# Performance work log

Measured on AMD Instinct MI355X. Metric: run time of the kernel, lower is better.

Reference implementation:

```python
import math
import jax, jax.numpy as jnp
import numpy as np

B, S, HID, NH = 2, 2048, 2048, 16
HD = HID // NH          # 128
QKD = HD // 2           # 64
BASE = 10000.0
LAYER_ID = 1
LAMBDA_INIT = 0.8 - 0.6 * math.exp(-0.3 * LAYER_ID)
EPS = 1e-6


def _rope_tables():
    i = np.arange(0, HD, 2, dtype=np.float32)
    theta = BASE ** (-i / HD)                      # [HD/2]
    pos = np.arange(S, dtype=np.float32)
    m_theta = np.outer(pos, theta)                 # [S, HD/2]
    cos = np.repeat(np.cos(m_theta), 2, axis=1)    # [S, HD]
    sin = np.repeat(np.sin(m_theta), 2, axis=1)
    return jnp.asarray(cos), jnp.asarray(sin)


def setup_inputs() -> dict:
    key = jax.random.key(0)
    ks = jax.random.split(key, 12)
    wstd = 0.02
    cos_emb, sin_emb = _rope_tables()
    return {
        "q": jax.random.normal(ks[0], (B, S, HID), jnp.float32),
        "k": jax.random.normal(ks[1], (B, S, HID), jnp.float32),
        "v": jax.random.normal(ks[2], (B, S, HID), jnp.float32),
        "Wq": jax.random.normal(ks[3], (HID, HID), jnp.float32) * wstd,
        "Wk": jax.random.normal(ks[4], (HID, HID), jnp.float32) * wstd,
        "Wv": jax.random.normal(ks[5], (HID, HID), jnp.float32) * wstd,
        "Wo": jax.random.normal(ks[6], (HID, HID), jnp.float32) * wstd,
        "lambda_q1": jax.random.normal(ks[7], (HD,), jnp.float32) * 0.1,
        "lambda_k1": jax.random.normal(ks[8], (HD,), jnp.float32) * 0.1,
        "lambda_q2": jax.random.normal(ks[9], (HD,), jnp.float32) * 0.1,
        "lambda_k2": jax.random.normal(ks[10], (HD,), jnp.float32) * 0.1,
        "gnorm_w": jnp.ones((HD,), jnp.float32),
        "cos_emb": cos_emb,
        "sin_emb": sin_emb,
        "mask": jnp.triu(jnp.ones((S, S), bool), 1),  # causal: True = masked
    }


def _apply_rope(x, cos_emb, sin_emb):
    # x: [B, 2, H, S, QKD]; tables sliced to [:S, :QKD] as in the torch code
    cos = cos_emb[:S, :QKD][None, None, None]
    sin = sin_emb[:S, :QKD][None, None, None]
    inv = jnp.stack((-x[..., 1::2], x[..., 0::2]), axis=-1).reshape(x.shape)
    return x * cos + inv * sin


def reference(q, k, v, Wq, Wk, Wv, Wo, lambda_q1, lambda_k1, lambda_q2,
              lambda_k2, gnorm_w, cos_emb, sin_emb, mask):
    lin = lambda x, W: jnp.einsum('bsi,oi->bso', x, W)  # torch Linear: x @ W.T
    qh = lin(q, Wq).reshape(B, S, NH, 2, QKD).transpose(0, 3, 2, 1, 4)  # [B,2,H,S,QKD]
    kh = lin(k, Wk).reshape(B, S, NH, 2, QKD).transpose(0, 3, 2, 1, 4)
    vh = lin(v, Wv).reshape(B, S, NH, HD).transpose(0, 2, 1, 3)          # [B,H,S,HD]
    qh = _apply_rope(qh, cos_emb, sin_emb)
    kh = _apply_rope(kh, cos_emb, sin_emb)

    scores = jnp.einsum('bghsd,bghtd->bghst', qh, kh) / math.sqrt(QKD)   # [B,2,H,S,S]
    scores = jnp.where(mask, jnp.finfo(jnp.float32).min, scores)

    lam1 = jnp.exp(jnp.sum(lambda_q1 * lambda_k1))
    lam2 = jnp.exp(jnp.sum(lambda_q2 * lambda_k2))
    lam = lam1 - lam2 + LAMBDA_INIT

    attn = jax.nn.softmax(scores[:, 0], axis=-1) - lam * jax.nn.softmax(scores[:, 1], axis=-1)
    out = jnp.einsum('bhst,bhtd->bhsd', attn, vh)                        # [B,H,S,HD]

    rms = out * jax.lax.rsqrt(jnp.mean(out * out, axis=-1, keepdims=True) + EPS) * gnorm_w
    out = (1.0 - LAMBDA_INIT) * rms
    out = out.transpose(0, 2, 1, 3).reshape(B, S, HID)
    return lin(out, Wo)
```

## Files before the change

kernel.cpp:

```cpp
#include <hip/hip_runtime.h>
#include <math.h>

#define BDIM 2
#define SDIM 2048
#define HIDD 2048
#define NHH 16
#define HDD 128
#define QKDD 64
#define MTOT (BDIM*SDIM)

constexpr float LAMBDA_INIT_F = 0.3555090675909693f;
constexpr float EPS_F = 1e-6f;
constexpr float SCALE_F = 0.125f;

typedef float f32x4 __attribute__((ext_vector_type(4)));
typedef short bf16x8 __attribute__((ext_vector_type(8)));
typedef short bf16x4 __attribute__((ext_vector_type(4)));

#define MFMA16(a, b, c) __builtin_amdgcn_mfma_f32_16x16x32_bf16((a), (b), (c), 0, 0, 0)

__device__ __forceinline__ short f2bf(float f) {
    unsigned u = __float_as_uint(f);
    u += 0x7FFFu + ((u >> 16) & 1u);
    return (short)(u >> 16);
}
__device__ __forceinline__ unsigned pk2(float a, float b) {
    return (unsigned)(unsigned short)f2bf(a) | ((unsigned)(unsigned short)f2bf(b) << 16);
}

__device__ __forceinline__ void gload_lds16(const void* g, void* l) {
    __builtin_amdgcn_global_load_lds(
        (const __attribute__((address_space(1))) void*)g,
        (__attribute__((address_space(3))) void*)l, 16, 0, 0);
}

__global__ void lambda_kernel(const float* __restrict__ lq1, const float* __restrict__ lk1,
                              const float* __restrict__ lq2, const float* __restrict__ lk2,
                              float* __restrict__ lam_out) {
    int l = threadIdx.x;
    float d1 = lq1[l] * lk1[l] + lq1[l + 64] * lk1[l + 64];
    float d2 = lq2[l] * lk2[l] + lq2[l + 64] * lk2[l + 64];
#pragma unroll
    for (int o = 32; o > 0; o >>= 1) {
        d1 += __shfl_down(d1, o);
        d2 += __shfl_down(d2, o);
    }
    if (l == 0) lam_out[0] = expf(d1) - expf(d2) + LAMBDA_INIT_F;
}

__global__ __launch_bounds__(256) void conv_x(const float* __restrict__ s0,
                                              const float* __restrict__ s1,
                                              const float* __restrict__ s2,
                                              short* __restrict__ dst, int n) {
    const float* src = (blockIdx.y == 0) ? s0 : (blockIdx.y == 1) ? s1 : s2;
    short* out = dst + (size_t)blockIdx.y * n;
    int i = (blockIdx.x * 256 + threadIdx.x) * 8;
    if (i >= n) return;
    float4 a = *(const float4*)&src[i];
    float4 b = *(const float4*)&src[i + 4];
    uint4 o;
    o.x = pk2(a.x, a.y); o.y = pk2(a.z, a.w);
    o.z = pk2(b.x, b.y); o.w = pk2(b.z, b.w);
    *(uint4*)&out[i] = o;
}
__global__ __launch_bounds__(256) void conv_w(const float* __restrict__ s0,
                                              const float* __restrict__ s1,
                                              const float* __restrict__ s2,
                                              const float* __restrict__ s3,
                                              short* __restrict__ dst, int n) {
    const float* src = (blockIdx.y == 0) ? s0 : (blockIdx.y == 1) ? s1
                     : (blockIdx.y == 2) ? s2 : s3;
    short* out = dst + (size_t)blockIdx.y * n;
    int i = (blockIdx.x * 256 + threadIdx.x) * 8;
    if (i >= n) return;
    float4 a = *(const float4*)&src[i];
    float4 b = *(const float4*)&src[i + 4];
    uint4 o;
    o.x = pk2(a.x, a.y); o.y = pk2(a.z, a.w);
    o.z = pk2(b.x, b.y); o.w = pk2(b.z, b.w);
    *(uint4*)&out[i] = o;
}

#define GK 2048

__device__ __forceinline__ void gemm_mainloop(
        const short* __restrict__ X, const short* __restrict__ W,
        short* As, short* Bs, f32x4 acc[4][4],
        int bm, int bn, int w, int l, int lq, int lg, int wr, int wc) {
    const int scol = (((l & 7) ^ (l >> 3)) << 3);
    const int rsw  = (lq & 7) << 3;
    const short* aS[4]; const short* bS[4];
    short* aD[4]; short* bD[4];
#pragma unroll
    for (int i = 0; i < 4; ++i) {
        const int c = w * 4 + i;
        aS[i] = X + (size_t)(bm + c * 8 + (l >> 3)) * GK + scol;
        bS[i] = W + (size_t)(bn + c * 8 + (l >> 3)) * GK + scol;
        aD[i] = As + c * 512;
        bD[i] = Bs + c * 512;
    }
    for (int k0 = 0; k0 < GK; k0 += 64) {
        __syncthreads();
#pragma unroll
        for (int i = 0; i < 4; ++i) {
            gload_lds16(aS[i] + k0, aD[i]);
            gload_lds16(bS[i] + k0, bD[i]);
        }
        __syncthreads();
#pragma unroll
        for (int kk = 0; kk < 2; ++kk) {
            bf16x8 a[4], b[4];
#pragma unroll
            for (int m = 0; m < 4; ++m)
                a[m] = *(const bf16x8*)&As[(wr * 64 + m * 16 + lq) * 64 + ((kk * 32 + lg * 8) ^ rsw)];
#pragma unroll
            for (int n = 0; n < 4; ++n)
                b[n] = *(const bf16x8*)&Bs[(wc * 64 + n * 16 + lq) * 64 + ((kk * 32 + lg * 8) ^ rsw)];
#pragma unroll
            for (int m = 0; m < 4; ++m)
#pragma unroll
                for (int n = 0; n < 4; ++n)
                    acc[m][n] = MFMA16(a[m], b[n], acc[m][n]);
        }
    }
}

__global__ __launch_bounds__(256) void qkv_gemm(
        const short* __restrict__ Xq, const short* __restrict__ Xk, const short* __restrict__ Xv,
        const short* __restrict__ Wb, short* __restrict__ Qb, short* __restrict__ Kb,
        short* __restrict__ Vb, const float* __restrict__ cosE, const float* __restrict__ sinE) {
    __shared__ short As[128 * 64];
    __shared__ short Bs[128 * 64];
    const int tid = threadIdx.x;
    const int w = tid >> 6, l = tid & 63;
    const int lq = l & 15, lg = l >> 4;
    const int wr = w >> 1, wc = w & 1;
    const int bm = blockIdx.y * 128;
    const int bn = blockIdx.x * 128;
    const int z  = blockIdx.z;

    const short* X = (z == 0) ? Xq : (z == 1) ? Xk : Xv;
    const short* W = Wb + (size_t)z * HIDD * HIDD;
    short* Cb      = (z == 0) ? Qb : (z == 1) ? Kb : Vb;

    f32x4 acc[4][4] = {};
    gemm_mainloop(X, W, As, Bs, acc, bm, bn, w, l, lq, lg, wr, wc);

    const bool dorope = (z < 2);
#pragma unroll
    for (int m = 0; m < 4; ++m)
#pragma unroll
        for (int n = 0; n < 4; ++n) {
            const int row0 = bm + wr * 64 + m * 16 + lg * 4;
            const int col  = bn + wc * 64 + n * 16 + lq;
#pragma unroll
            for (int r = 0; r < 4; ++r) {
                float vv = acc[m][n][r];
                if (dorope) {
                    const int s  = (row0 + r) & (SDIM - 1);
                    const int c6 = col & 63;
                    const float cv = cosE[s * HDD + c6];
                    const float sv = sinE[s * HDD + c6];
                    const float p = __shfl_xor(vv, 1);
                    vv = (col & 1) ? vv * cv + p * sv : vv * cv - p * sv;
                }
                Cb[(size_t)(row0 + r) * HIDD + col] = f2bf(vv);
            }
        }
}

__global__ __launch_bounds__(256) void o_gemm(const short* __restrict__ Ab,
                                              const short* __restrict__ Bb,
                                              float* __restrict__ C) {
    __shared__ short As[128 * 64];
    __shared__ short Bs[128 * 64];
    const int tid = threadIdx.x;
    const int w = tid >> 6, l = tid & 63;
    const int lq = l & 15, lg = l >> 4;
    const int wr = w >> 1, wc = w & 1;
    const int bm = blockIdx.y * 128;
    const int bn = blockIdx.x * 128;

    f32x4 acc[4][4] = {};
    gemm_mainloop(Ab, Bb, As, Bs, acc, bm, bn, w, l, lq, lg, wr, wc);

#pragma unroll
    for (int m = 0; m < 4; ++m)
#pragma unroll
        for (int n = 0; n < 4; ++n) {
            const int row0 = bm + wr * 64 + m * 16 + lg * 4;
            const int col  = bn + wc * 64 + n * 16 + lq;
#pragma unroll
            for (int r = 0; r < 4; ++r)
                C[(size_t)(row0 + r) * HIDD + col] = acc[m][n][r];
        }
}

#define KVB 64

__device__ __forceinline__ bf16x8 pack_pa(const float p0[4], const float p1[4]) {
    union { unsigned u[4]; bf16x8 v; } r;
    r.u[0] = pk2(p0[0], p0[1]);
    r.u[1] = pk2(p0[2], p0[3]);
    r.u[2] = pk2(p1[0], p1[1]);
    r.u[3] = pk2(p1[2], p1[3]);
    return r.v;
}

__device__ __forceinline__ void softmax_step(
        f32x4 sc[4], float& M, float& L, f32x4 O[8], bf16x8 pa[2],
        int t0, int qg, int lg, bool domask) {
#pragma unroll
    for (int sub = 0; sub < 4; ++sub)
#pragma unroll
        for (int r = 0; r < 4; ++r) {
            float s = sc[sub][r] * SCALE_F;
            if (domask) {
                int key = t0 + sub * 16 + lg * 4 + r;
                s = (key <= qg) ? s : -1e30f;
            }
            sc[sub][r] = s;
        }
    float mx = -1e30f;
#pragma unroll
    for (int sub = 0; sub < 4; ++sub) {
        float a01 = fmaxf(sc[sub][0], sc[sub][1]);
        float a23 = fmaxf(sc[sub][2], sc[sub][3]);
        mx = fmaxf(mx, fmaxf(a01, a23));
    }
    mx = fmaxf(mx, __shfl_xor(mx, 16));
    mx = fmaxf(mx, __shfl_xor(mx, 32));
    if (__ballot(mx > M + 8.f)) {
        const float Mn = fmaxf(M, mx);
        const float a = __expf(M - Mn);
        M = Mn;
        L *= a;
        float ar[4];
#pragma unroll
        for (int r = 0; r < 4; ++r) ar[r] = __shfl(a, lg * 4 + r);
#pragma unroll
        for (int d = 0; d < 8; ++d) {
            O[d][0] *= ar[0]; O[d][1] *= ar[1]; O[d][2] *= ar[2]; O[d][3] *= ar[3];
        }
    }
    float p[4][4];
    float ps = 0.f;
#pragma unroll
    for (int sub = 0; sub < 4; ++sub) {
#pragma unroll
        for (int r = 0; r < 4; ++r) p[sub][r] = __expf(sc[sub][r] - M);
        ps += (p[sub][0] + p[sub][1]) + (p[sub][2] + p[sub][3]);
    }
    ps += __shfl_xor(ps, 16);
    ps += __shfl_xor(ps, 32);
    L += ps;
    pa[0] = pack_pa(p[0], p[1]);
    pa[1] = pack_pa(p[2], p[3]);
}

__global__ __launch_bounds__(256, 2) void flash_mfma(
        const short* __restrict__ Qb, const short* __restrict__ Kb,
        const short* __restrict__ Vb, const float* __restrict__ gnw,
        const float* __restrict__ lam_p, short* __restrict__ Hob) {
    __shared__ short Ksh[KVB * 128];
    __shared__ short VT[HDD * 72];

    const int tid = threadIdx.x;
    const int w  = tid >> 6;
    const int l  = tid & 63;
    const int lq = l & 15;
    const int lg = l >> 4;

    const int blk = blockIdx.x;
    const int bh  = blk & 31;
    const int bx  = 31 - (blk >> 5);
    const int b = bh >> 4, h = bh & 15;
    const int s0 = bx * 64;
    const float lam = lam_p[0];

    const int qg = s0 + w * 16 + lq;
    const short* qrow = Qb + ((size_t)(b * SDIM + qg)) * HIDD + h * HDD;
    bf16x8 qf[2][2];
#pragma unroll
    for (int br = 0; br < 2; ++br)
#pragma unroll
        for (int ks = 0; ks < 2; ++ks)
            qf[br][ks] = *(const bf16x8*)(qrow + br * 64 + ks * 32 + lg * 8);

    int kkey[4], kcol[4];
#pragma unroll
    for (int i = 0; i < 4; ++i) {
        kkey[i] = w * 16 + i * 4 + lg;
        kcol[i] = (lq * 8) ^ ((kkey[i] & 7) << 3);
    }
    const int kp = tid & 31, dq = tid >> 5;

    const short* Kbase = Kb + ((size_t)(b * SDIM)) * HIDD + h * HDD;
    const short* Vbase = Vb + ((size_t)(b * SDIM)) * HIDD + h * HDD;

    float M1 = -1e30f, M2 = -1e30f, L1 = 0.f, L2 = 0.f;
    f32x4 O1[8] = {}; f32x4 O2[8] = {};

    const int ntmax = bx + 1;
    const int qmin = s0 + w * 16;
    const int ntw = (qmin >> 6) + 1;

    for (int t = 0; t < ntmax; ++t) {
        const size_t trow = (size_t)t * KVB * HIDD;
        __syncthreads();
#pragma unroll
        for (int i = 0; i < 4; ++i)
            gload_lds16(Kbase + trow + (size_t)kkey[i] * HIDD + kcol[i],
                        &Ksh[w * 2048 + i * 512]);
        {
            const short* v0 = Vbase + trow + (size_t)(2 * kp) * HIDD + dq * 16;
            const short* v1 = v0 + HIDD;
            bf16x8 v00 = *(const bf16x8*)v0;
            bf16x8 v01 = *(const bf16x8*)(v0 + 8);
            bf16x8 v10 = *(const bf16x8*)v1;
            bf16x8 v11 = *(const bf16x8*)(v1 + 8);
#pragma unroll
            for (int j = 0; j < 8; ++j) {
                unsigned ua = (unsigned)(unsigned short)v00[j] |
                              ((unsigned)(unsigned short)v10[j] << 16);
                *(unsigned*)&VT[(dq * 16 + j) * 72 + 2 * kp] = ua;
                unsigned ub = (unsigned)(unsigned short)v01[j] |
                              ((unsigned)(unsigned short)v11[j] << 16);
                *(unsigned*)&VT[(dq * 16 + 8 + j) * 72 + 2 * kp] = ub;
            }
        }
        __syncthreads();
        if (t >= ntw) continue;

        f32x4 sc1[4] = {}; f32x4 sc2[4] = {};
        const int rsw = (lq & 7) << 3;
#pragma unroll
        for (int sub = 0; sub < 4; ++sub) {
            const int rbase = (sub * 16 + lq) * 128;
            bf16x8 k00 = *(const bf16x8*)&Ksh[rbase + ((lg * 8) ^ rsw)];
            bf16x8 k01 = *(const bf16x8*)&Ksh[rbase + ((32 + lg * 8) ^ rsw)];
            bf16x8 k10 = *(const bf16x8*)&Ksh[rbase + ((64 + lg * 8) ^ rsw)];
            bf16x8 k11 = *(const bf16x8*)&Ksh[rbase + ((96 + lg * 8) ^ rsw)];
            sc1[sub] = MFMA16(k00, qf[0][0], sc1[sub]);
            sc1[sub] = MFMA16(k01, qf[0][1], sc1[sub]);
            sc2[sub] = MFMA16(k10, qf[1][0], sc2[sub]);
            sc2[sub] = MFMA16(k11, qf[1][1], sc2[sub]);
        }
        const int t0 = t * KVB;
        const bool domask = (t0 + KVB - 1 > qmin);
        bf16x8 pa1[2], pa2[2];
        softmax_step(sc1, M1, L1, O1, pa1, t0, qg, lg, domask);
        softmax_step(sc2, M2, L2, O2, pa2, t0, qg, lg, domask);

#pragma unroll
        for (int d0 = 0; d0 < 8; ++d0) {
            const short* vrow = &VT[(d0 * 16 + lq) * 72];
            bf16x4 a0 = *(const bf16x4*)&vrow[lg * 4];
            bf16x4 a1 = *(const bf16x4*)&vrow[16 + lg * 4];
            bf16x4 b0 = *(const bf16x4*)&vrow[32 + lg * 4];
            bf16x4 b1 = *(const bf16x4*)&vrow[48 + lg * 4];
            bf16x8 vb0 = __builtin_shufflevector(a0, a1, 0, 1, 2, 3, 4, 5, 6, 7);
            bf16x8 vb1 = __builtin_shufflevector(b0, b1, 0, 1, 2, 3, 4, 5, 6, 7);
            O1[d0] = MFMA16(pa1[0], vb0, O1[d0]);
            O1[d0] = MFMA16(pa1[1], vb1, O1[d0]);
            O2[d0] = MFMA16(pa2[0], vb0, O2[d0]);
            O2[d0] = MFMA16(pa2[1], vb1, O2[d0]);
        }
    }

    const float inv1 = 1.f / L1;
    const float inv2 = lam / L2;
    float i1[4], i2[4];
#pragma unroll
    for (int r = 0; r < 4; ++r) {
        i1[r] = __shfl(inv1, lg * 4 + r);
        i2[r] = __shfl(inv2, lg * 4 + r);
    }
    float gn[8];
#pragma unroll
    for (int d = 0; d < 8; ++d) gn[d] = gnw[d * 16 + lq];
    float od[8][4];
    float ss[4] = {0.f, 0.f, 0.f, 0.f};
#pragma unroll
    for (int d = 0; d < 8; ++d)
#pragma unroll
        for (int r = 0; r < 4; ++r) {
            float o = O1[d][r] * i1[r] - O2[d][r] * i2[r];
            od[d][r] = o;
            ss[r] += o * o;
        }
#pragma unroll
    for (int r = 0; r < 4; ++r) {
        ss[r] += __shfl_xor(ss[r], 1);
        ss[r] += __shfl_xor(ss[r], 2);
        ss[r] += __shfl_xor(ss[r], 4);
        ss[r] += __shfl_xor(ss[r], 8);
    }
#pragma unroll
    for (int r = 0; r < 4; ++r) {
        const float scal = rsqrtf(ss[r] * (1.0f / HDD) + EPS_F) * (1.0f - LAMBDA_INIT_F);
        const size_t orow = ((size_t)(b * SDIM + s0 + w * 16 + lg * 4 + r)) * HIDD + h * HDD;
#pragma unroll
        for (int d = 0; d < 8; ++d)
            Hob[orow + d * 16 + lq] = f2bf(od[d][r] * scal * gn[d]);
    }
}

extern "C" void kernel_launch(void* const* d_in, const int* in_sizes, int n_in,
                              void* d_out, int out_size, void* d_ws, size_t ws_size,
                              hipStream_t stream) {
    const float* q   = (const float*)d_in[0];
    const float* k   = (const float*)d_in[1];
    const float* v   = (const float*)d_in[2];
    const float* Wq  = (const float*)d_in[3];
    const float* Wk  = (const float*)d_in[4];
    const float* Wv  = (const float*)d_in[5];
    const float* Wo  = (const float*)d_in[6];
    const float* lq1 = (const float*)d_in[7];
    const float* lk1 = (const float*)d_in[8];
    const float* lq2 = (const float*)d_in[9];
    const float* lk2 = (const float*)d_in[10];
    const float* gnw = (const float*)d_in[11];
    const float* cosE = (const float*)d_in[12];
    const float* sinE = (const float*)d_in[13];
    float* out = (float*)d_out;

    const size_t TEN = (size_t)BDIM * SDIM * HIDD;
    const int   WN  = HIDD * HIDD;

    short* wsS = (short*)d_ws;
    short* Qb   = wsS;
    short* Kb   = wsS + TEN;
    short* Vb   = wsS + 2 * TEN;
    short* xqkv = wsS + 3 * TEN;
    short* wb4  = wsS + 6 * TEN;
    float* lamp = (float*)(wsS + 6 * TEN + (size_t)4 * WN);
    short* Hob  = xqkv;

    lambda_kernel<<<1, 64, 0, stream>>>(lq1, lk1, lq2, lk2, lamp);

    dim3 gx((int)(TEN / 8 / 256), 3);
    conv_x<<<gx, 256, 0, stream>>>(q, k, v, xqkv, (int)TEN);
    dim3 gw(WN / 8 / 256, 4);
    conv_w<<<gw, 256, 0, stream>>>(Wq, Wk, Wv, Wo, wb4, WN);

    dim3 gq(HIDD / 128, MTOT / 128, 3);
    qkv_gemm<<<gq, 256, 0, stream>>>(xqkv, xqkv + TEN, xqkv + 2 * TEN, wb4,
                                     Qb, Kb, Vb, cosE, sinE);

    flash_mfma<<<(SDIM / 64) * BDIM * NHH, 256, 0, stream>>>(Qb, Kb, Vb, gnw, lamp, Hob);

    dim3 go(HIDD / 128, MTOT / 128);
    o_gemm<<<go, 256, 0, stream>>>(Hob, wb4 + (size_t)3 * WN, out);
}
```

Baseline: 330.6 us.

## Double-buffer GEMM LDS tiles with async prefetch and raise MFMA priority in attention

Rewrites the shared GEMM mainloop as a two-stage LDS double buffer. The next K tile is issued with global_load_lds while the current tile's MFMAs run, and explicit vmcnt/lgkmcnt waits plus raw barriers replace the two __syncthreads per iteration. It also wraps the attention kernel's MFMA sections in s_setprio so matrix work is favoured over other waves. This doubles LDS per block, which can lower occupancy, and the hand-written waitcnt and barrier ordering risks subtle races.

```diff
diff --git a/kernel.cpp b/kernel.cpp
--- a/kernel.cpp
+++ b/kernel.cpp
@@ -33,6 +33,11 @@
         (const __attribute__((address_space(1))) void*)g,
         (__attribute__((address_space(3))) void*)l, 16, 0, 0);
 }
+__device__ __forceinline__ void waitv8() { asm volatile("s_waitcnt vmcnt(8)" ::: "memory"); }
+__device__ __forceinline__ void waitv0() { asm volatile("s_waitcnt vmcnt(0)" ::: "memory"); }
+__device__ __forceinline__ void waitl0() { asm volatile("s_waitcnt lgkmcnt(0)" ::: "memory"); }
+#define SBAR()   __builtin_amdgcn_s_barrier()
+#define SCHEDB() __builtin_amdgcn_sched_barrier(0)
 
 __global__ void lambda_kernel(const float* __restrict__ lq1, const float* __restrict__ lk1,
                               const float* __restrict__ lq2, const float* __restrict__ lk2,
@@ -90,38 +95,108 @@
     const int scol = (((l & 7) ^ (l >> 3)) << 3);
     const int rsw  = (lq & 7) << 3;
     const short* aS[4]; const short* bS[4];
-    short* aD[4]; short* bD[4];
 #pragma unroll
     for (int i = 0; i < 4; ++i) {
         const int c = w * 4 + i;
         aS[i] = X + (size_t)(bm + c * 8 + (l >> 3)) * GK + scol;
         bS[i] = W + (size_t)(bn + c * 8 + (l >> 3)) * GK + scol;
-        aD[i] = As + c * 512;
-        bD[i] = Bs + c * 512;
-    }
-    for (int k0 = 0; k0 < GK; k0 += 64) {
-        __syncthreads();
-#pragma unroll
-        for (int i = 0; i < 4; ++i) {
-            gload_lds16(aS[i] + k0, aD[i]);
-            gload_lds16(bS[i] + k0, bD[i]);
-        }
-        __syncthreads();
-#pragma unroll
-        for (int kk = 0; kk < 2; ++kk) {
-            bf16x8 a[4], b[4];
+    }
+    const int dOff = (w * 4) * 512;
+
+#pragma unroll
+    for (int i = 0; i < 4; ++i) {
+        gload_lds16(aS[i], As + dOff + i * 512);
+        gload_lds16(bS[i], Bs + dOff + i * 512);
+    }
+#pragma unroll
+    for (int i = 0; i < 4; ++i) {
+        gload_lds16(aS[i] + 64, As + 8192 + dOff + i * 512);
+        gload_lds16(bS[i] + 64, Bs + 8192 + dOff + i * 512);
+    }
+    waitv8();
+    SBAR();
+
+    for (int t = 0; t < 30; ++t) {
+        const short* Ab = As + (t & 1) * 8192;
+        const short* Bb = Bs + (t & 1) * 8192;
+        bf16x8 a[4][2], b[4][2];
+#pragma unroll
+        for (int m = 0; m < 4; ++m)
+#pragma unroll
+            for (int kk = 0; kk < 2; ++kk)
+                a[m][kk] = *(const bf16x8*)&Ab[(wr * 64 + m * 16 + lq) * 64 + ((kk * 32 + lg * 8) ^ rsw)];
+#pragma unroll
+        for (int n = 0; n < 4; ++n)
+#pragma unroll
+            for (int kk = 0; kk < 2; ++kk)
+                b[n][kk] = *(const bf16x8*)&Bb[(wc * 64 + n * 16 + lq) * 64 + ((kk * 32 + lg * 8) ^ rsw)];
+        waitl0(); SCHEDB();
+        SBAR();
+        {
+            short* Ad = As + (t & 1) * 8192 + dOff;
+            short* Bd = Bs + (t & 1) * 8192 + dOff;
+            const short* aK = aS[0] + (t + 2) * 64;
+            (void)aK;
+#pragma unroll
+            for (int i = 0; i < 4; ++i) {
+                gload_lds16(aS[i] + (t + 2) * 64, Ad + i * 512);
+                gload_lds16(bS[i] + (t + 2) * 64, Bd + i * 512);
+            }
+        }
+        SCHEDB();
+#pragma unroll
+        for (int kk = 0; kk < 2; ++kk)
 #pragma unroll
             for (int m = 0; m < 4; ++m)
-                a[m] = *(const bf16x8*)&As[(wr * 64 + m * 16 + lq) * 64 + ((kk * 32 + lg * 8) ^ rsw)];
-#pragma unroll
-            for (int n = 0; n < 4; ++n)
-                b[n] = *(const bf16x8*)&Bs[(wc * 64 + n * 16 + lq) * 64 + ((kk * 32 + lg * 8) ^ rsw)];
+#pragma unroll
+                for (int n = 0; n < 4; ++n)
+                    acc[m][n] = MFMA16(a[m][kk], b[n][kk], acc[m][n]);
+        waitv8();
+        SBAR();
+    }
+    {
+        bf16x8 a[4][2], b[4][2];
+#pragma unroll
+        for (int m = 0; m < 4; ++m)
+#pragma unroll
+            for (int kk = 0; kk < 2; ++kk)
+                a[m][kk] = *(const bf16x8*)&As[(wr * 64 + m * 16 + lq) * 64 + ((kk * 32 + lg * 8) ^ rsw)];
+#pragma unroll
+        for (int n = 0; n < 4; ++n)
+#pragma unroll
+            for (int kk = 0; kk < 2; ++kk)
+                b[n][kk] = *(const bf16x8*)&Bs[(wc * 64 + n * 16 + lq) * 64 + ((kk * 32 + lg * 8) ^ rsw)];
+        waitl0(); SCHEDB();
+        SBAR();
+#pragma unroll
+        for (int kk = 0; kk < 2; ++kk)
 #pragma unroll
             for (int m = 0; m < 4; ++m)
 #pragma unroll
                 for (int n = 0; n < 4; ++n)
-                    acc[m][n] = MFMA16(a[m], b[n], acc[m][n]);
-        }
+                    acc[m][n] = MFMA16(a[m][kk], b[n][kk], acc[m][n]);
+        waitv0();
+        SBAR();
+    }
+    {
+        bf16x8 a[4][2], b[4][2];
+#pragma unroll
+        for (int m = 0; m < 4; ++m)
+#pragma unroll
+            for (int kk = 0; kk < 2; ++kk)
+                a[m][kk] = *(const bf16x8*)&As[8192 + (wr * 64 + m * 16 + lq) * 64 + ((kk * 32 + lg * 8) ^ rsw)];
+#pragma unroll
+        for (int n = 0; n < 4; ++n)
+#pragma unroll
+            for (int kk = 0; kk < 2; ++kk)
+                b[n][kk] = *(const bf16x8*)&Bs[8192 + (wc * 64 + n * 16 + lq) * 64 + ((kk * 32 + lg * 8) ^ rsw)];
+#pragma unroll
+        for (int kk = 0; kk < 2; ++kk)
+#pragma unroll
+            for (int m = 0; m < 4; ++m)
+#pragma unroll
+                for (int n = 0; n < 4; ++n)
+                    acc[m][n] = MFMA16(a[m][kk], b[n][kk], acc[m][n]);
     }
 }
 
@@ -129,8 +204,8 @@
         const short* __restrict__ Xq, const short* __restrict__ Xk, const short* __restrict__ Xv,
         const short* __restrict__ Wb, short* __restrict__ Qb, short* __restrict__ Kb,
         short* __restrict__ Vb, const float* __restrict__ cosE, const float* __restrict__ sinE) {
-    __shared__ short As[128 * 64];
-    __shared__ short Bs[128 * 64];
+    __shared__ short As[2 * 128 * 64];
+    __shared__ short Bs[2 * 128 * 64];
     const int tid = threadIdx.x;
     const int w = tid >> 6, l = tid & 63;
     const int lq = l & 15, lg = l >> 4;
@@ -172,8 +247,8 @@
 __global__ __launch_bounds__(256) void o_gemm(const short* __restrict__ Ab,
                                               const short* __restrict__ Bb,
                                               float* __restrict__ C) {
-    __shared__ short As[128 * 64];
-    __shared__ short Bs[128 * 64];
+    __shared__ short As[2 * 128 * 64];
+    __shared__ short Bs[2 * 128 * 64];
     const int tid = threadIdx.x;
     const int w = tid >> 6, l = tid & 63;
     const int lq = l & 15, lg = l >> 4;
@@ -334,6 +409,7 @@
 
         f32x4 sc1[4] = {}; f32x4 sc2[4] = {};
         const int rsw = (lq & 7) << 3;
+        __builtin_amdgcn_s_setprio(1);
 #pragma unroll
         for (int sub = 0; sub < 4; ++sub) {
             const int rbase = (sub * 16 + lq) * 128;
@@ -346,12 +422,14 @@
             sc2[sub] = MFMA16(k10, qf[1][0], sc2[sub]);
             sc2[sub] = MFMA16(k11, qf[1][1], sc2[sub]);
         }
+        __builtin_amdgcn_s_setprio(0);
         const int t0 = t * KVB;
         const bool domask = (t0 + KVB - 1 > qmin);
         bf16x8 pa1[2], pa2[2];
         softmax_step(sc1, M1, L1, O1, pa1, t0, qg, lg, domask);
         softmax_step(sc2, M2, L2, O2, pa2, t0, qg, lg, domask);
 
+        __builtin_amdgcn_s_setprio(1);
 #pragma unroll
         for (int d0 = 0; d0 < 8; ++d0) {
             const short* vrow = &VT[(d0 * 16 + lq) * 72];
@@ -366,6 +444,7 @@
             O2[d0] = MFMA16(pa2[0], vb0, O2[d0]);
             O2[d0] = MFMA16(pa2[1], vb1, O2[d0]);
         }
+        __builtin_amdgcn_s_setprio(0);
     }
 
     const float inv1 = 1.f / L1;
```

Result: faster. 314.8 us (-4.8%).
